# Performance work log

Hardware: AMD Instinct MI355X
Metric: run time of the kernel (lower is better)

The kernel has to match this reference:

```python
import jax, jax.numpy as jnp
import numpy as np

B, K, D = 16384, 20, 256
H = 4                    # attention heads
DECAY = 0.95
THRESH = 2.0             # anomaly z-score threshold
EPS = 1e-8


def setup_inputs() -> dict:
    key = jax.random.key(0)
    ks = jax.random.split(key, 10)
    s = 0.05
    return {
        "storage": jax.random.normal(ks[0], (B, K, D), jnp.float32),
        "new_message": jax.random.normal(ks[1], (B, D), jnp.float32),
        "ad_w1": jax.random.normal(ks[2], (D // 2, D), jnp.float32) * s,
        "ad_b1": jnp.zeros((D // 2,), jnp.float32),
        "ad_w2": jax.random.normal(ks[3], (1, D // 2), jnp.float32) * s,
        "ad_b2": jnp.zeros((1,), jnp.float32),
        "imp_w1": jax.random.normal(ks[4], (D, 2 * D), jnp.float32) * s,
        "imp_b1": jnp.zeros((D,), jnp.float32),
        "imp_w2": jax.random.normal(ks[5], (1, D), jnp.float32) * s,
        "imp_b2": jnp.zeros((1,), jnp.float32),
        "attn_in_w": jax.random.normal(ks[6], (3 * D, D), jnp.float32) * s,
        "attn_in_b": jnp.zeros((3 * D,), jnp.float32),
        "attn_out_w": jax.random.normal(ks[7], (D, D), jnp.float32) * s,
        "attn_out_b": jnp.zeros((D,), jnp.float32),
    }


def reference(storage, new_message, ad_w1, ad_b1, ad_w2, ad_b2,
              imp_w1, imp_b1, imp_w2, imp_b2,
              attn_in_w, attn_in_b, attn_out_w, attn_out_b):
    dt = storage.dtype
    b = storage.shape[0]
    # --- masked historical statistics over the storage slots ---
    mask = (jnp.sum(jnp.abs(storage), axis=-1) > 0).astype(dt)          # [B,K]
    denom = jnp.sum(mask, axis=1, keepdims=True) + EPS                  # [B,1]
    hmean = jnp.sum(storage * mask[..., None], axis=1) / denom          # [B,D]
    diff_sq = ((storage - hmean[:, None, :]) ** 2) * mask[..., None]
    hstd = jnp.sqrt(jnp.sum(diff_sq, axis=1) / denom)                   # [B,D]
    # --- anomaly score: statistical z-score + learned detector ---
    z = jnp.abs((new_message - hmean) / (hstd + EPS))
    stat_anom = jnp.mean((z > THRESH).astype(dt), axis=-1, keepdims=True)  # [B,1]
    h = jax.nn.relu(new_message @ ad_w1.T + ad_b1)
    learned_anom = jax.nn.sigmoid(h @ ad_w2.T + ad_b2)                  # [B,1]
    anomaly = 0.5 * stat_anom + 0.5 * learned_anom
    # --- importance weight ---
    ctx = jnp.concatenate([new_message, hmean], axis=-1)                # [B,2D]
    imp = jax.nn.softplus(jax.nn.relu(ctx @ imp_w1.T + imp_b1) @ imp_w2.T + imp_b2)
    imp = imp * (1.0 + anomaly)                                         # [B,1]
    # --- decay, roll, scatter-insert new message ---
    decay = (DECAY ** jnp.arange(K, dtype=dt))[None, :, None]           # [1,K,1]
    st = storage * decay
    st = jnp.roll(st, shift=1, axis=1)
    st = st.at[:, 0, :].set(new_message * imp)                          # [B,K,D]
    # --- multihead attention: query=new_message, key/value=storage ---
    wq, wk, wv = jnp.split(attn_in_w, 3, axis=0)
    bq, bk, bv = jnp.split(attn_in_b, 3)
    hd = D // H
    q = (new_message @ wq.T + bq).reshape(b, 1, H, hd)
    k = (st @ wk.T + bk).reshape(b, K, H, hd)
    v = (st @ wv.T + bv).reshape(b, K, H, hd)
    scores = jnp.einsum('bqhd,bkhd->bhqk', q, k) / jnp.sqrt(jnp.asarray(hd, dt))
    attn = jax.nn.softmax(scores, axis=-1)                              # [B,H,1,K]
    ctx_out = jnp.einsum('bhqk,bkhd->bqhd', attn, v).reshape(b, 1, D)
    agg = (ctx_out @ attn_out_w.T + attn_out_b)[:, 0, :]                # [B,D]
    return st, agg
```

## Files before the change

### kernel.cpp

```cpp
#include <hip/hip_runtime.h>
#include <hip/hip_bf16.h>
#include <math.h>

#define B_N 16384
#define K_N 20
#define D_N 256
#define H_N 4

typedef __attribute__((ext_vector_type(8))) short v8s;
typedef __attribute__((ext_vector_type(4))) float v4f;
typedef __hip_bfloat16 bf16;

static __device__ __forceinline__ float bf2f(bf16 x){ return __bfloat162float(x); }
static __device__ __forceinline__ bf16 f2bf(float x){ return __float2bfloat16(x); }
static __device__ __forceinline__ float bfb2f(short s){ bf16 v; *(short*)&v = s; return __bfloat162float(v); }
static __device__ __forceinline__ short bfbits(float x){ bf16 v = __float2bfloat16(x); return *(short*)&v; }

__global__ __launch_bounds__(256) void k_prep(
    const float* __restrict__ ad_w1, const float* __restrict__ ad_b1,
    const float* __restrict__ imp_w1, const float* __restrict__ imp_b1,
    const float* __restrict__ attn_in_w, const float* __restrict__ attn_in_b,
    const float* __restrict__ attn_out_w, const float* __restrict__ nm,
    bf16* __restrict__ attn_bf, bf16* __restrict__ impw1_bf, bf16* __restrict__ wout_bf,
    bf16* __restrict__ wcat, float* __restrict__ catb,
    float* __restrict__ g, float* __restrict__ qc,
    bf16* __restrict__ wkT, bf16* __restrict__ nm_bf)
{
    long o = (long)blockIdx.x * 256 + threadIdx.x;
    const long n_attn = 768*256, n_imp = 256*512, n_wout = 256*256, n_wcat = 640*256;
    const long n_catb = 640, n_g = 1024, n_qc = 4, n_wkT = 1024*64, n_nm = (long)B_N*256;
    if (o < n_attn){ attn_bf[o] = f2bf(attn_in_w[o]); return; } o -= n_attn;
    if (o < n_imp){ impw1_bf[o] = f2bf(imp_w1[o]); return; } o -= n_imp;
    if (o < n_wout){ wout_bf[o] = f2bf(attn_out_w[o]); return; } o -= n_wout;
    if (o < n_wcat){
        int r = (int)(o >> 8), c = (int)(o & 255); float v;
        if (r < 128)      v = ad_w1[r*256 + c];
        else if (r < 384) v = attn_in_w[(r-128)*256 + c];
        else              v = imp_w1[(r-384)*512 + c];
        wcat[o] = f2bf(v); return; } o -= n_wcat;
    if (o < n_catb){
        int r = (int)o; float v;
        if (r < 128) v = ad_b1[r]; else if (r < 384) v = attn_in_b[r-128]; else v = imp_b1[r-384];
        catb[r] = v; return; } o -= n_catb;
    if (o < n_g){
        int h = (int)(o >> 8), d = (int)(o & 255); float s = 0.f;
        for (int j = 0; j < 64; ++j) s += attn_in_w[(h*64+j)*256 + d] * attn_in_b[256 + h*64 + j];
        g[o] = s; return; } o -= n_g;
    if (o < n_qc){
        int h = (int)o; float s = 0.f;
        for (int j = 0; j < 64; ++j) s += attn_in_b[h*64+j] * attn_in_b[256 + h*64 + j];
        qc[h] = s; return; } o -= n_qc;
    if (o < n_wkT){
        int c = (int)(o >> 6), i = (int)(o & 63);
        int h = c >> 8, d = c & 255;
        wkT[o] = f2bf(attn_in_w[(256 + h*64 + i)*256 + d]); return; } o -= n_wkT;
    if (o < n_nm){ nm_bf[o] = f2bf(nm[o]); return; }
}

__global__ __launch_bounds__(256) void k_stats(const float* __restrict__ storage,
    const float* __restrict__ nm, bf16* __restrict__ hmean_bf, float* __restrict__ stat_anom)
{
    int b = blockIdx.x, t = threadIdx.x, wave = t >> 6;
    const float* S = storage + (long)b * K_N * D_N;
    float x[K_N];
    #pragma unroll
    for (int k = 0; k < K_N; ++k) x[k] = S[k*D_N + t];
    __shared__ int wnz[K_N][4];
    __shared__ int cnts[4];
    #pragma unroll
    for (int k = 0; k < K_N; ++k){
        unsigned long long bal = __ballot(x[k] != 0.0f);
        if ((t & 63) == 0) wnz[k][wave] = (bal != 0ULL) ? 1 : 0;
    }
    __syncthreads();
    float cm = 0.f, s1 = 0.f, s2 = 0.f;
    #pragma unroll
    for (int k = 0; k < K_N; ++k){
        float m = (wnz[k][0] | wnz[k][1] | wnz[k][2] | wnz[k][3]) ? 1.0f : 0.0f;
        cm += m; s1 += m * x[k]; s2 += m * x[k] * x[k];
    }
    float denom = cm + 1e-8f;
    float mu = s1 / denom;
    float var = (s2 - 2.0f*mu*s1 + mu*mu*cm) / denom;
    float sd = sqrtf(fmaxf(var, 0.0f));
    hmean_bf[(long)b*D_N + t] = f2bf(mu);
    float z = fabsf((nm[(long)b*D_N + t] - mu) / (sd + 1e-8f));
    unsigned long long bal = __ballot(z > 2.0f);
    if ((t & 63) == 0) cnts[wave] = __popcll(bal);
    __syncthreads();
    if (t == 0) stat_anom[b] = (float)(cnts[0]+cnts[1]+cnts[2]+cnts[3]) * (1.0f/256.0f);
}

__global__ __launch_bounds__(256) void k_gemm(
    const bf16* __restrict__ X, int ldx, int agshift, int agstride,
    const bf16* __restrict__ W, int ldw,
    const float* __restrict__ bias,
    const bf16* __restrict__ csrc, int ldc,
    void* __restrict__ outp, int ldo, int out_bf16,
    int relu_hi, int Kd)
{
    int wave = threadIdx.x >> 6, lane = threadIdx.x & 63;
    int l15 = lane & 15, koct = lane >> 4;
    int rblk = blockIdx.x * 64 + wave * 16;
    int cb = blockIdx.y * 64;
    long arow = rblk + l15;
    long aoff = (long)(cb >> agshift) * agstride;
    const bf16* Xp = X + arow * ldx + aoff + koct * 8;
    v4f acc[4];
    #pragma unroll
    for (int ct = 0; ct < 4; ++ct) acc[ct] = (v4f){0.f,0.f,0.f,0.f};
    for (int k0 = 0; k0 < Kd; k0 += 32){
        v8s a = *(const v8s*)(Xp + k0);
        #pragma unroll
        for (int ct = 0; ct < 4; ++ct){
            const bf16* Wp = W + (long)(cb + ct*16 + l15) * ldw + k0 + koct * 8;
            v8s bb = *(const v8s*)Wp;
            acc[ct] = __builtin_amdgcn_mfma_f32_16x16x32_bf16(a, bb, acc[ct], 0, 0, 0);
        }
    }
    int orow_base = rblk + koct * 4;
    #pragma unroll
    for (int ct = 0; ct < 4; ++ct){
        int ocol = cb + ct*16 + l15;
        float bv = bias ? bias[ocol] : 0.0f;
        #pragma unroll
        for (int r = 0; r < 4; ++r){
            long orow = orow_base + r;
            float v = acc[ct][r] + bv;
            if (csrc) v += bf2f(csrc[orow * ldc + ocol]);
            if (ocol < relu_hi) v = fmaxf(v, 0.0f);
            if (out_bf16) ((bf16*)outp)[orow * ldo + ocol] = f2bf(v);
            else          ((float*)outp)[orow * ldo + ocol] = v;
        }
    }
}

__global__ __launch_bounds__(256) void k_learned(const bf16* __restrict__ cat1,
    const float* __restrict__ ad_w2, const float* __restrict__ ad_b2, float* __restrict__ learned)
{
    int wave = threadIdx.x >> 6, lane = threadIdx.x & 63;
    long b = (long)blockIdx.x * 4 + wave;
    float p = 0.f;
    #pragma unroll
    for (int m = 0; m < 2; ++m){ int j = lane + 64*m; p += bf2f(cat1[b*640 + j]) * ad_w2[j]; }
    #pragma unroll
    for (int s = 32; s; s >>= 1) p += __shfl_xor(p, s);
    if (lane == 0) learned[b] = 1.0f / (1.0f + expf(-(p + ad_b2[0])));
}

__global__ __launch_bounds__(256) void k_imp(const bf16* __restrict__ t_bf,
    const float* __restrict__ imp_w2, const float* __restrict__ imp_b2,
    const float* __restrict__ stat_anom, const float* __restrict__ learned, float* __restrict__ imp)
{
    int wave = threadIdx.x >> 6, lane = threadIdx.x & 63;
    long b = (long)blockIdx.x * 4 + wave;
    float p = 0.f;
    #pragma unroll
    for (int m = 0; m < 4; ++m){ int j = lane + 64*m; p += bf2f(t_bf[b*256 + j]) * imp_w2[j]; }
    #pragma unroll
    for (int s = 32; s; s >>= 1) p += __shfl_xor(p, s);
    if (lane == 0){
        float x = p + imp_b2[0];
        float sp = (x > 20.0f) ? x : log1pf(expf(x));
        float an = 0.5f * stat_anom[b] + 0.5f * learned[b];
        imp[b] = sp * (1.0f + an);
    }
}

__global__ __launch_bounds__(256) void k_attn(const float* __restrict__ storage,
    const float* __restrict__ nm, const bf16* __restrict__ R_bf, const float* __restrict__ imp,
    const float* __restrict__ g, const float* __restrict__ qc,
    float* __restrict__ st_out, bf16* __restrict__ u_bf)
{
    __shared__ float4 stor4[(K_N-1) * 64];
    int b = blockIdx.x, t = threadIdx.x, h = t >> 6, lane = t & 63;
    const float4* S4 = (const float4*)(storage + (long)b * K_N * D_N);
    float4*       O4 = (float4*)(st_out + (long)b * K_N * D_N);

    float impv = imp[b];
    float4 nm4 = ((const float4*)(nm + (long)b * D_N))[lane];
    short4 r4  = ((const short4*)(R_bf + (long)b * (H_N*D_N) + h * D_N))[lane];
    float4 R4;
    R4.x = bfb2f(r4.x); R4.y = bfb2f(r4.y); R4.z = bfb2f(r4.z); R4.w = bfb2f(r4.w);
    float4 g4 = ((const float4*)(g + h * D_N))[lane];
    float qch = qc[h];

    float4 vv[5];
    #pragma unroll
    for (int j = 0; j < 5; ++j){
        int i = t + j*256;
        if (i < (K_N-1)*64) vv[j] = S4[i];
    }
    {
        float dd = 1.0f;
        int r0 = t >> 6;
        #pragma unroll
        for (int j = 0; j < 3; ++j) if (j < r0) dd *= 0.95f;
        const float step = 0.81450625f;
        #pragma unroll
        for (int j = 0; j < 5; ++j){
            int i = t + j*256;
            if (i < (K_N-1)*64){
                stor4[i] = vv[j];
                float4 o;
                o.x = vv[j].x * dd; o.y = vv[j].y * dd;
                o.z = vv[j].z * dd; o.w = vv[j].w * dd;
                O4[i + 64] = o;
            }
            dd *= step;
        }
    }
    if (h == 0){
        float4 o;
        o.x = impv * nm4.x; o.y = impv * nm4.y;
        o.z = impv * nm4.z; o.w = impv * nm4.w;
        O4[lane] = o;
    }
    __syncthreads();

    const int NP = K_N + 1;
    float p[NP];
    p[0] = nm4.x*g4.x + nm4.y*g4.y + nm4.z*g4.z + nm4.w*g4.w;
    p[1] = nm4.x*R4.x + nm4.y*R4.y + nm4.z*R4.z + nm4.w*R4.w;
    #pragma unroll
    for (int k = 0; k < K_N-1; ++k){
        float4 x = stor4[k*64 + lane];
        p[2+k] = x.x*R4.x + x.y*R4.y + x.z*R4.z + x.w*R4.w;
    }
    #pragma unroll
    for (int s = 32; s; s >>= 1){
        #pragma unroll
        for (int j = 0; j < NP; ++j) p[j] += __shfl_xor(p[j], s);
    }
    float dec[K_N-1];
    dec[0] = 1.0f;
    #pragma unroll
    for (int k = 1; k < K_N-1; ++k) dec[k] = dec[k-1] * 0.95f;
    float qb = p[0] + qch;
    float sc[K_N];
    sc[0] = (impv * p[1] + qb) * 0.125f;
    #pragma unroll
    for (int k = 0; k < K_N-1; ++k) sc[k+1] = (dec[k] * p[2+k] + qb) * 0.125f;
    float mx = sc[0];
    #pragma unroll
    for (int k = 1; k < K_N; ++k) mx = fmaxf(mx, sc[k]);
    float l = 0.f, w[K_N];
    #pragma unroll
    for (int k = 0; k < K_N; ++k){ w[k] = expf(sc[k]-mx); l += w[k]; }
    float inv = 1.0f / l;
    float w0 = w[0] * inv * impv;
    float cw[K_N-1];
    #pragma unroll
    for (int k = 0; k < K_N-1; ++k) cw[k] = w[k+1] * inv * dec[k];

    float4 acc;
    acc.x = w0 * nm4.x; acc.y = w0 * nm4.y; acc.z = w0 * nm4.z; acc.w = w0 * nm4.w;
    #pragma unroll
    for (int k = 0; k < K_N-1; ++k){
        float4 x = stor4[k*64 + lane];
        acc.x += cw[k]*x.x; acc.y += cw[k]*x.y; acc.z += cw[k]*x.z; acc.w += cw[k]*x.w;
    }
    short4 us;
    us.x = bfbits(acc.x); us.y = bfbits(acc.y); us.z = bfbits(acc.z); us.w = bfbits(acc.w);
    ((short4*)(u_bf + (long)b * (H_N*D_N) + h * D_N))[lane] = us;
}

extern "C" void kernel_launch(void* const* d_in, const int* in_sizes, int n_in,
                              void* d_out, int out_size, void* d_ws, size_t ws_size,
                              hipStream_t stream)
{
    (void)in_sizes; (void)n_in; (void)out_size; (void)ws_size;
    const float* storage    = (const float*)d_in[0];
    const float* nm         = (const float*)d_in[1];
    const float* ad_w1      = (const float*)d_in[2];
    const float* ad_b1      = (const float*)d_in[3];
    const float* ad_w2      = (const float*)d_in[4];
    const float* ad_b2      = (const float*)d_in[5];
    const float* imp_w1     = (const float*)d_in[6];
    const float* imp_b1     = (const float*)d_in[7];
    const float* imp_w2     = (const float*)d_in[8];
    const float* imp_b2     = (const float*)d_in[9];
    const float* attn_in_w  = (const float*)d_in[10];
    const float* attn_in_b  = (const float*)d_in[11];
    const float* attn_out_w = (const float*)d_in[12];
    const float* attn_out_b = (const float*)d_in[13];

    char* p = (char*)d_ws;
    auto alloc = [&](size_t bytes)->char*{ char* r = p; p += (bytes + 255) & ~(size_t)255; return r; };
    bf16*  attn_bf   = (bf16*) alloc((size_t)768*256*2);
    bf16*  impw1_bf  = (bf16*) alloc((size_t)256*512*2);
    bf16*  wout_bf   = (bf16*) alloc((size_t)256*256*2);
    bf16*  wcat      = (bf16*) alloc((size_t)640*256*2);
    float* catb      = (float*)alloc((size_t)640*4);
    float* g         = (float*)alloc((size_t)1024*4);
    float* qc        = (float*)alloc((size_t)4*4);
    bf16*  wkT       = (bf16*) alloc((size_t)1024*64*2);
    bf16*  nm_bf     = (bf16*) alloc((size_t)B_N*256*2);
    bf16*  hmean_bf  = (bf16*) alloc((size_t)B_N*256*2);
    float* stat_anom = (float*)alloc((size_t)B_N*4);
    bf16*  cat1      = (bf16*) alloc((size_t)B_N*640*2);
    float* learned   = (float*)alloc((size_t)B_N*4);
    bf16*  R_bf      = (bf16*) alloc((size_t)B_N*1024*2);
    bf16*  t_bf      = (bf16*) alloc((size_t)B_N*256*2);
    float* imp       = (float*)alloc((size_t)B_N*4);
    bf16*  u_bf      = (bf16*) alloc((size_t)B_N*1024*2);
    bf16*  ctx_bf    = (bf16*) alloc((size_t)B_N*256*2);

    float* st_out  = (float*)d_out;
    float* agg_out = (float*)d_out + (size_t)B_N * K_N * D_N;

    {
        long total = 768*256 + 256*512 + 256*256 + 640*256 + 640 + 1024 + 4 + 1024*64 + (long)B_N*256;
        int grid = (int)((total + 255) / 256);
        k_prep<<<grid, 256, 0, stream>>>(ad_w1, ad_b1, imp_w1, imp_b1, attn_in_w, attn_in_b,
                                         attn_out_w, nm, attn_bf, impw1_bf, wout_bf, wcat, catb,
                                         g, qc, wkT, nm_bf);
    }
    k_stats<<<B_N, 256, 0, stream>>>(storage, nm, hmean_bf, stat_anom);
    k_gemm<<<dim3(B_N/64, 640/64), 256, 0, stream>>>(nm_bf, 256, 30, 0, wcat, 256, catb,
        (const bf16*)nullptr, 0, cat1, 640, 1, 128, 256);
    k_learned<<<B_N/4, 256, 0, stream>>>(cat1, ad_w2, ad_b2, learned);
    k_gemm<<<dim3(B_N/64, 1024/64), 256, 0, stream>>>(cat1 + 128, 640, 8, 64, wkT, 64,
        (const float*)nullptr, (const bf16*)nullptr, 0, R_bf, 1024, 1, 0, 64);
    k_gemm<<<dim3(B_N/64, 256/64), 256, 0, stream>>>(hmean_bf, 256, 30, 0, impw1_bf + 256, 512,
        (const float*)nullptr, cat1 + 384, 640, t_bf, 256, 1, 256, 256);
    k_imp<<<B_N/4, 256, 0, stream>>>(t_bf, imp_w2, imp_b2, stat_anom, learned, imp);
    k_attn<<<B_N, 256, 0, stream>>>(storage, nm, R_bf, imp, g, qc, st_out, u_bf);
    k_gemm<<<dim3(B_N/64, 256/64), 256, 0, stream>>>(u_bf, 1024, 6, 256, attn_bf + 512*256, 256,
        attn_in_b + 512, (const bf16*)nullptr, 0, ctx_bf, 256, 1, 0, 256);
    k_gemm<<<dim3(B_N/64, 256/64), 256, 0, stream>>>(ctx_bf, 256, 30, 0, wout_bf, 256,
        attn_out_b, (const bf16*)nullptr, 0, agg_out, 256, 0, 0, 256);
}
```

Measured before the change: 880.2 us.

## Fuse stats, importance MLP and anomaly heads into the attention kernel

Removes the separate stats, learned-anomaly, importance GEMM and importance kernels, computing masked mean/std, z-score count, the hmean half of the importance MLP, and both scalar heads inside the per-row attention kernel. Storage is read once into shared memory instead of twice, and the intermediate hmean, t, learned and imp buffers plus four launches go away. In exchange, the hmean×W1 product becomes a per-thread scalar dot product that streams a bf16 weight row from cache for every batch row, instead of running as an MFMA GEMM. It also adds block-level syncs and more shared memory.

```diff
diff --git a/kernel.cpp b/kernel.cpp
--- a/kernel.cpp
+++ b/kernel.cpp
@@ -21,16 +21,18 @@
     const float* __restrict__ imp_w1, const float* __restrict__ imp_b1,
     const float* __restrict__ attn_in_w, const float* __restrict__ attn_in_b,
     const float* __restrict__ attn_out_w, const float* __restrict__ nm,
-    bf16* __restrict__ attn_bf, bf16* __restrict__ impw1_bf, bf16* __restrict__ wout_bf,
+    bf16* __restrict__ attn_bf, bf16* __restrict__ w1b, bf16* __restrict__ wout_bf,
     bf16* __restrict__ wcat, float* __restrict__ catb,
     float* __restrict__ g, float* __restrict__ qc,
     bf16* __restrict__ wkT, bf16* __restrict__ nm_bf)
 {
     long o = (long)blockIdx.x * 256 + threadIdx.x;
-    const long n_attn = 768*256, n_imp = 256*512, n_wout = 256*256, n_wcat = 640*256;
+    const long n_attn = 768*256, n_w1b = 65536, n_wout = 256*256, n_wcat = 640*256;
     const long n_catb = 640, n_g = 1024, n_qc = 4, n_wkT = 1024*64, n_nm = (long)B_N*256;
     if (o < n_attn){ attn_bf[o] = f2bf(attn_in_w[o]); return; } o -= n_attn;
-    if (o < n_imp){ impw1_bf[o] = f2bf(imp_w1[o]); return; } o -= n_imp;
+    if (o < n_w1b){
+        int j = (int)(o >> 8), k = (int)(o & 255);
+        w1b[o] = f2bf(imp_w1[j*512 + 256 + k]); return; } o -= n_w1b;
     if (o < n_wout){ wout_bf[o] = f2bf(attn_out_w[o]); return; } o -= n_wout;
     if (o < n_wcat){
         int r = (int)(o >> 8), c = (int)(o & 255); float v;
@@ -57,40 +59,6 @@
     if (o < n_nm){ nm_bf[o] = f2bf(nm[o]); return; }
 }
 
-__global__ __launch_bounds__(256) void k_stats(const float* __restrict__ storage,
-    const float* __restrict__ nm, bf16* __restrict__ hmean_bf, float* __restrict__ stat_anom)
-{
-    int b = blockIdx.x, t = threadIdx.x, wave = t >> 6;
-    const float* S = storage + (long)b * K_N * D_N;
-    float x[K_N];
-    #pragma unroll
-    for (int k = 0; k < K_N; ++k) x[k] = S[k*D_N + t];
-    __shared__ int wnz[K_N][4];
-    __shared__ int cnts[4];
-    #pragma unroll
-    for (int k = 0; k < K_N; ++k){
-        unsigned long long bal = __ballot(x[k] != 0.0f);
-        if ((t & 63) == 0) wnz[k][wave] = (bal != 0ULL) ? 1 : 0;
-    }
-    __syncthreads();
-    float cm = 0.f, s1 = 0.f, s2 = 0.f;
-    #pragma unroll
-    for (int k = 0; k < K_N; ++k){
-        float m = (wnz[k][0] | wnz[k][1] | wnz[k][2] | wnz[k][3]) ? 1.0f : 0.0f;
-        cm += m; s1 += m * x[k]; s2 += m * x[k] * x[k];
-    }
-    float denom = cm + 1e-8f;
-    float mu = s1 / denom;
-    float var = (s2 - 2.0f*mu*s1 + mu*mu*cm) / denom;
-    float sd = sqrtf(fmaxf(var, 0.0f));
-    hmean_bf[(long)b*D_N + t] = f2bf(mu);
-    float z = fabsf((nm[(long)b*D_N + t] - mu) / (sd + 1e-8f));
-    unsigned long long bal = __ballot(z > 2.0f);
-    if ((t & 63) == 0) cnts[wave] = __popcll(bal);
-    __syncthreads();
-    if (t == 0) stat_anom[b] = (float)(cnts[0]+cnts[1]+cnts[2]+cnts[3]) * (1.0f/256.0f);
-}
-
 __global__ __launch_bounds__(256) void k_gemm(
     const bf16* __restrict__ X, int ldx, int agshift, int agstride,
     const bf16* __restrict__ W, int ldw,
@@ -135,49 +103,25 @@
     }
 }
 
-__global__ __launch_bounds__(256) void k_learned(const bf16* __restrict__ cat1,
-    const float* __restrict__ ad_w2, const float* __restrict__ ad_b2, float* __restrict__ learned)
-{
-    int wave = threadIdx.x >> 6, lane = threadIdx.x & 63;
-    long b = (long)blockIdx.x * 4 + wave;
-    float p = 0.f;
-    #pragma unroll
-    for (int m = 0; m < 2; ++m){ int j = lane + 64*m; p += bf2f(cat1[b*640 + j]) * ad_w2[j]; }
-    #pragma unroll
-    for (int s = 32; s; s >>= 1) p += __shfl_xor(p, s);
-    if (lane == 0) learned[b] = 1.0f / (1.0f + expf(-(p + ad_b2[0])));
-}
-
-__global__ __launch_bounds__(256) void k_imp(const bf16* __restrict__ t_bf,
+__global__ __launch_bounds__(256) void k_fused(
+    const float* __restrict__ storage, const float* __restrict__ nm,
+    const bf16* __restrict__ R_bf, const bf16* __restrict__ cat1,
+    const bf16* __restrict__ w1b,
+    const float* __restrict__ ad_w2, const float* __restrict__ ad_b2,
     const float* __restrict__ imp_w2, const float* __restrict__ imp_b2,
-    const float* __restrict__ stat_anom, const float* __restrict__ learned, float* __restrict__ imp)
-{
-    int wave = threadIdx.x >> 6, lane = threadIdx.x & 63;
-    long b = (long)blockIdx.x * 4 + wave;
-    float p = 0.f;
-    #pragma unroll
-    for (int m = 0; m < 4; ++m){ int j = lane + 64*m; p += bf2f(t_bf[b*256 + j]) * imp_w2[j]; }
-    #pragma unroll
-    for (int s = 32; s; s >>= 1) p += __shfl_xor(p, s);
-    if (lane == 0){
-        float x = p + imp_b2[0];
-        float sp = (x > 20.0f) ? x : log1pf(expf(x));
-        float an = 0.5f * stat_anom[b] + 0.5f * learned[b];
-        imp[b] = sp * (1.0f + an);
-    }
-}
-
-__global__ __launch_bounds__(256) void k_attn(const float* __restrict__ storage,
-    const float* __restrict__ nm, const bf16* __restrict__ R_bf, const float* __restrict__ imp,
     const float* __restrict__ g, const float* __restrict__ qc,
     float* __restrict__ st_out, bf16* __restrict__ u_bf)
 {
-    __shared__ float4 stor4[(K_N-1) * 64];
+    __shared__ float4 stor4[K_N * 64];
+    __shared__ float nm_s[D_N];
+    __shared__ float mu_s[D_N];
+    __shared__ float mask_s[K_N];
+    __shared__ int   zc_s[H_N];
+    __shared__ float red_s[2*H_N];
     int b = blockIdx.x, t = threadIdx.x, h = t >> 6, lane = t & 63;
     const float4* S4 = (const float4*)(storage + (long)b * K_N * D_N);
     float4*       O4 = (float4*)(st_out + (long)b * K_N * D_N);
 
-    float impv = imp[b];
     float4 nm4 = ((const float4*)(nm + (long)b * D_N))[lane];
     short4 r4  = ((const short4*)(R_bf + (long)b * (H_N*D_N) + h * D_N))[lane];
     float4 R4;
@@ -187,21 +131,22 @@
 
     float4 vv[5];
     #pragma unroll
-    for (int j = 0; j < 5; ++j){
-        int i = t + j*256;
-        if (i < (K_N-1)*64) vv[j] = S4[i];
-    }
+    for (int j = 0; j < 5; ++j) vv[j] = S4[t + j*256];
+    if (h == 0) ((float4*)nm_s)[lane] = nm4;
     {
         float dd = 1.0f;
-        int r0 = t >> 6;
-        #pragma unroll
-        for (int j = 0; j < 3; ++j) if (j < r0) dd *= 0.95f;
+        #pragma unroll
+        for (int j = 0; j < 3; ++j) if (j < h) dd *= 0.95f;
         const float step = 0.81450625f;
         #pragma unroll
         for (int j = 0; j < 5; ++j){
             int i = t + j*256;
-            if (i < (K_N-1)*64){
-                stor4[i] = vv[j];
+            int row = h + 4*j;
+            stor4[i] = vv[j];
+            bool nz = (vv[j].x != 0.f) || (vv[j].y != 0.f) || (vv[j].z != 0.f) || (vv[j].w != 0.f);
+            unsigned long long bal = __ballot(nz);
+            if (lane == 0) mask_s[row] = (bal != 0ULL) ? 1.0f : 0.0f;
+            if (row < K_N-1){
                 float4 o;
                 o.x = vv[j].x * dd; o.y = vv[j].y * dd;
                 o.z = vv[j].z * dd; o.w = vv[j].w * dd;
@@ -210,13 +155,63 @@
             dd *= step;
         }
     }
+    __syncthreads();
+
+    {
+        const float* S = (const float*)stor4;
+        float cm = 0.f, s1 = 0.f, s2 = 0.f;
+        #pragma unroll
+        for (int k = 0; k < K_N; ++k){
+            float m = mask_s[k];
+            float x = S[k*D_N + t];
+            cm += m; s1 += m*x; s2 += m*x*x;
+        }
+        float denom = cm + 1e-8f;
+        float mu = s1 / denom;
+        float var = (s2 - 2.0f*mu*s1 + mu*mu*cm) / denom;
+        float sd = sqrtf(fmaxf(var, 0.0f));
+        mu_s[t] = mu;
+        float z = fabsf((nm_s[t] - mu) / (sd + 1e-8f));
+        unsigned long long bal = __ballot(z > 2.0f);
+        if (lane == 0) zc_s[h] = __popcll(bal);
+    }
+    __syncthreads();
+
+    {
+        float acc = bf2f(cat1[(long)b*640 + 384 + t]);
+        const v8s* wrow = (const v8s*)(w1b + (long)t * 256);
+        const float4* mu4 = (const float4*)mu_s;
+        #pragma unroll
+        for (int c = 0; c < 32; ++c){
+            v8s wv8 = wrow[c];
+            float4 ma = mu4[2*c], mb = mu4[2*c+1];
+            acc += ma.x*bfb2f(wv8[0]) + ma.y*bfb2f(wv8[1]) + ma.z*bfb2f(wv8[2]) + ma.w*bfb2f(wv8[3])
+                 + mb.x*bfb2f(wv8[4]) + mb.y*bfb2f(wv8[5]) + mb.z*bfb2f(wv8[6]) + mb.w*bfb2f(wv8[7]);
+        }
+        float tj = fmaxf(acc, 0.0f);
+        float pi = tj * imp_w2[t];
+        float pl = (t < 128) ? bf2f(cat1[(long)b*640 + t]) * ad_w2[t] : 0.0f;
+        #pragma unroll
+        for (int s = 32; s; s >>= 1){ pi += __shfl_xor(pi, s); pl += __shfl_xor(pl, s); }
+        if (lane == 0){ red_s[h] = pi; red_s[H_N + h] = pl; }
+    }
+    __syncthreads();
+
+    float impv;
+    {
+        float p  = red_s[0]+red_s[1]+red_s[2]+red_s[3] + imp_b2[0];
+        float plr= red_s[4]+red_s[5]+red_s[6]+red_s[7] + ad_b2[0];
+        float learned = 1.0f / (1.0f + expf(-plr));
+        float stat = (float)(zc_s[0]+zc_s[1]+zc_s[2]+zc_s[3]) * (1.0f/256.0f);
+        float sp = (p > 20.0f) ? p : log1pf(expf(p));
+        impv = sp * (1.0f + 0.5f*stat + 0.5f*learned);
+    }
     if (h == 0){
         float4 o;
         o.x = impv * nm4.x; o.y = impv * nm4.y;
         o.z = impv * nm4.z; o.w = impv * nm4.w;
         O4[lane] = o;
     }
-    __syncthreads();
 
     const int NP = K_N + 1;
     float p[NP];
@@ -288,7 +283,7 @@
     char* p = (char*)d_ws;
     auto alloc = [&](size_t bytes)->char*{ char* r = p; p += (bytes + 255) & ~(size_t)255; return r; };
     bf16*  attn_bf   = (bf16*) alloc((size_t)768*256*2);
-    bf16*  impw1_bf  = (bf16*) alloc((size_t)256*512*2);
+    bf16*  w1b       = (bf16*) alloc((size_t)256*256*2);
     bf16*  wout_bf   = (bf16*) alloc((size_t)256*256*2);
     bf16*  wcat      = (bf16*) alloc((size_t)640*256*2);
     float* catb      = (float*)alloc((size_t)640*4);
@@ -296,13 +291,8 @@
     float* qc        = (float*)alloc((size_t)4*4);
     bf16*  wkT       = (bf16*) alloc((size_t)1024*64*2);
     bf16*  nm_bf     = (bf16*) alloc((size_t)B_N*256*2);
-    bf16*  hmean_bf  = (bf16*) alloc((size_t)B_N*256*2);
-    float* stat_anom = (float*)alloc((size_t)B_N*4);
     bf16*  cat1      = (bf16*) alloc((size_t)B_N*640*2);
-    float* learned   = (float*)alloc((size_t)B_N*4);
     bf16*  R_bf      = (bf16*) alloc((size_t)B_N*1024*2);
-    bf16*  t_bf      = (bf16*) alloc((size_t)B_N*256*2);
-    float* imp       = (float*)alloc((size_t)B_N*4);
     bf16*  u_bf      = (bf16*) alloc((size_t)B_N*1024*2);
     bf16*  ctx_bf    = (bf16*) alloc((size_t)B_N*256*2);
 
@@ -310,22 +300,18 @@
     float* agg_out = (float*)d_out + (size_t)B_N * K_N * D_N;
 
     {
-        long total = 768*256 + 256*512 + 256*256 + 640*256 + 640 + 1024 + 4 + 1024*64 + (long)B_N*256;
+        long total = 768*256 + 65536 + 256*256 + 640*256 + 640 + 1024 + 4 + 1024*64 + (long)B_N*256;
         int grid = (int)((total + 255) / 256);
         k_prep<<<grid, 256, 0, stream>>>(ad_w1, ad_b1, imp_w1, imp_b1, attn_in_w, attn_in_b,
-                                         attn_out_w, nm, attn_bf, impw1_bf, wout_bf, wcat, catb,
+                                         attn_out_w, nm, attn_bf, w1b, wout_bf, wcat, catb,
                                          g, qc, wkT, nm_bf);
     }
-    k_stats<<<B_N, 256, 0, stream>>>(storage, nm, hmean_bf, stat_anom);
     k_gemm<<<dim3(B_N/64, 640/64), 256, 0, stream>>>(nm_bf, 256, 30, 0, wcat, 256, catb,
         (const bf16*)nullptr, 0, cat1, 640, 1, 128, 256);
-    k_learned<<<B_N/4, 256, 0, stream>>>(cat1, ad_w2, ad_b2, learned);
     k_gemm<<<dim3(B_N/64, 1024/64), 256, 0, stream>>>(cat1 + 128, 640, 8, 64, wkT, 64,
         (const float*)nullptr, (const bf16*)nullptr, 0, R_bf, 1024, 1, 0, 64);
-    k_gemm<<<dim3(B_N/64, 256/64), 256, 0, stream>>>(hmean_bf, 256, 30, 0, impw1_bf + 256, 512,
-        (const float*)nullptr, cat1 + 384, 640, t_bf, 256, 1, 256, 256);
-    k_imp<<<B_N/4, 256, 0, stream>>>(t_bf, imp_w2, imp_b2, stat_anom, learned, imp);
-    k_attn<<<B_N, 256, 0, stream>>>(storage, nm, R_bf, imp, g, qc, st_out, u_bf);
+    k_fused<<<B_N, 256, 0, stream>>>(storage, nm, R_bf, cat1, w1b,
+        ad_w2, ad_b2, imp_w2, imp_b2, g, qc, st_out, u_bf);
     k_gemm<<<dim3(B_N/64, 256/64), 256, 0, stream>>>(u_bf, 1024, 6, 256, attn_bf + 512*256, 256,
         attn_in_b + 512, (const bf16*)nullptr, 0, ctx_bf, 256, 1, 0, 256);
     k_gemm<<<dim3(B_N/64, 256/64), 256, 0, stream>>>(ctx_bf, 256, 30, 0, wout_bf, 256,
```

Result: slower. 1.295 ms (+47.1%).
